# Kernel tuning notes

Measured on AMD Instinct MI355X. Metric: run time of the kernel, lower is better.

The kernel has to match this reference:

```python
import jax, jax.numpy as jnp
import numpy as np
import math

HID = 2048; NH = 16; NKV = 4; NG = NH // NKV
LORA = 512; D_ROPE = 64; D_NOPE = 128; D_V = 128
D_QK = D_NOPE + D_ROPE  # 192
B, S = 2, 2048
ROPE_BASE = 10000.0


def setup_inputs() -> dict:
    key = jax.random.key(0)
    ks = jax.random.split(key, 5)
    s = lambda fan_in: 1.0 / math.sqrt(fan_in)
    return {
        "hidden_states": jax.random.normal(ks[0], (B, S, HID), jnp.float32),
        "Wqkv": jax.random.uniform(ks[1], (HID, NH * D_QK + LORA), jnp.float32, -s(HID), s(HID)),
        "Wk_up": jax.random.uniform(ks[2], (LORA, NKV * D_QK), jnp.float32, -s(LORA), s(LORA)),
        "Wv_up": jax.random.uniform(ks[3], (LORA, NKV * D_V), jnp.float32, -s(LORA), s(LORA)),
        "Wo": jax.random.uniform(ks[4], (NH * D_V, HID), jnp.float32, -s(NH * D_V), s(NH * D_V)),
    }


def _rope(x, seq_len):
    # x: [b, s, h, D_ROPE]; standard rotate-half RoPE
    inv_freq = 1.0 / (ROPE_BASE ** (jnp.arange(0, D_ROPE, 2, dtype=jnp.float32) / D_ROPE))
    t = jnp.arange(seq_len, dtype=jnp.float32)
    freqs = jnp.outer(t, inv_freq)                      # [s, D_ROPE/2]
    emb = jnp.concatenate([freqs, freqs], axis=-1)      # [s, D_ROPE]
    cos = jnp.cos(emb)[None, :, None, :].astype(x.dtype)
    sin = jnp.sin(emb)[None, :, None, :].astype(x.dtype)
    x1, x2 = jnp.split(x, 2, axis=-1)
    rot = jnp.concatenate([-x2, x1], axis=-1)
    return x * cos + rot * sin


def reference(hidden_states, Wqkv, Wk_up, Wv_up, Wo):
    b, s, _ = hidden_states.shape
    qkv = hidden_states @ Wqkv                              # [b,s,NH*D_QK+LORA]
    q, c_kv = jnp.split(qkv, [NH * D_QK], axis=-1)
    q = q.reshape(b, s, NH, D_QK)
    k = (c_kv @ Wk_up).reshape(b, s, NKV, D_QK)
    v = (c_kv @ Wv_up).reshape(b, s, NKV, D_V)
    q_nope, q_rope = jnp.split(q, [D_NOPE], axis=-1)
    k_nope, k_rope = jnp.split(k, [D_NOPE], axis=-1)
    q = jnp.concatenate([q_nope, _rope(q_rope, s)], axis=-1)   # [b,s,NH,D_QK]
    k = jnp.concatenate([k_nope, _rope(k_rope, s)], axis=-1)   # [b,s,NKV,D_QK]
    # GQA broadcast: repeat_interleave kv heads to NH
    k = jnp.repeat(k, NG, axis=2)
    v = jnp.repeat(v, NG, axis=2)
    scale = 1.0 / math.sqrt(D_QK)
    scores = jnp.einsum("bqhd,bkhd->bhqk", q, k) * scale
    causal = jnp.tril(jnp.ones((s, s), bool))
    scores = jnp.where(causal[None, None], scores, jnp.finfo(scores.dtype).min)
    probs = jax.nn.softmax(scores, axis=-1)
    out = jnp.einsum("bhqk,bkhd->bqhd", probs, v).reshape(b, s, NH * D_V)
    return out @ Wo
```

## Files before the change

### kernel.cpp

```cpp
#include <hip/hip_runtime.h>
#include <hip/hip_bf16.h>
#include <math.h>

#define HIDN  2048
#define NH    16
#define NKV   4
#define LORA  512
#define D_ROPE 64
#define D_NOPE 128
#define D_VV  128
#define D_QKD 192
#define BATCH 2
#define SEQ   2048
#define NTOK  (BATCH*SEQ)
#define QKV_W (NH*D_QKD + LORA)
#define KW    (NKV*D_QKD)
#define VW    (NKV*D_VV)
#define AW    (NH*D_VV)
#define QSCALE 0.07216878364870323f
#define LOG2E  1.4426950408889634f

typedef __attribute__((ext_vector_type(8))) __bf16 bf16x8;
typedef __attribute__((ext_vector_type(4))) float f32x4;

static __device__ __forceinline__ unsigned short f2bf(float f) {
    unsigned int u = __builtin_bit_cast(unsigned int, f);
    u += 0x7fffu + ((u >> 16) & 1u);
    return (unsigned short)(u >> 16);
}
static __device__ __forceinline__ float bf2f(unsigned short v) {
    unsigned int u = (unsigned int)v << 16;
    return __builtin_bit_cast(float, u);
}
static __device__ __forceinline__ unsigned int cvt_pk_bf16(float lo, float hi) {
    unsigned int r;
    asm("v_cvt_pk_bf16_f32 %0, %1, %2" : "=v"(r) : "v"(lo), "v"(hi));
    return r;
}
static __device__ __forceinline__ void gl2lds16(const unsigned short* g, unsigned short* l) {
    __builtin_amdgcn_global_load_lds(
        (const __attribute__((address_space(1))) unsigned int*)g,
        (__attribute__((address_space(3))) unsigned int*)l, 16, 0, 0);
}

__global__ __launch_bounds__(256) void transpose_w(
    const float* __restrict__ W, unsigned short* __restrict__ Wt,
    int K, int N, int scale_ncols, float scale)
{
    __shared__ float T[64][68];
    const int tid = threadIdx.x;
    const int k0 = blockIdx.y * 64, n0 = blockIdx.x * 64;
    const int rr = tid >> 4;
    const int c4 = (tid & 15) * 4;

#pragma unroll
    for (int i = 0; i < 4; ++i) {
        int r = rr + 16 * i;
        *(float4*)&T[r][c4] = *(const float4*)&W[(size_t)(k0 + r) * N + n0 + c4];
    }
    __syncthreads();
#pragma unroll
    for (int i = 0; i < 4; ++i) {
        int nr = rr + 16 * i;
        float sc = (n0 + nr < scale_ncols) ? scale : 1.0f;
        unsigned short tmp[4];
#pragma unroll
        for (int j = 0; j < 4; ++j) tmp[j] = f2bf(T[c4 + j][nr] * sc);
        unsigned int p0 = (unsigned int)tmp[0] | ((unsigned int)tmp[1] << 16);
        unsigned int p1 = (unsigned int)tmp[2] | ((unsigned int)tmp[3] << 16);
        *(uint2*)&Wt[(size_t)(n0 + nr) * K + k0 + c4] = make_uint2(p0, p1);
    }
}

__global__ __launch_bounds__(256) void cast_plain(const float* __restrict__ src,
                                                  unsigned short* __restrict__ dst)
{
    int idx = blockIdx.x * 256 + threadIdx.x;
    float4 v = *(const float4*)&src[(size_t)idx * 4];
    unsigned int p0 = (unsigned int)f2bf(v.x) | ((unsigned int)f2bf(v.y) << 16);
    unsigned int p1 = (unsigned int)f2bf(v.z) | ((unsigned int)f2bf(v.w) << 16);
    *(uint2*)&dst[(size_t)idx * 4] = make_uint2(p0, p1);
}

template<int OUT_MODE>
__global__ __launch_bounds__(256) void gemm_bt(
    const unsigned short* __restrict__ A,
    const unsigned short* __restrict__ Bt,
    void* __restrict__ C,
    int K, int lda, int ldb, int ldc)
{
    __shared__ __align__(16) unsigned short As[128 * 32];
    __shared__ __align__(16) unsigned short Bs[128 * 32];

    const int tid  = threadIdx.x;
    const int w    = tid >> 6;
    const int lane = tid & 63;
    const int quad = lane >> 4;
    const int l15  = lane & 15;
    const int brow = blockIdx.y * 128;
    const int bcol = blockIdx.x * 128;
    const int wr   = (w >> 1) * 64;
    const int wc   = (w & 1) * 64;

    const int srow = lane >> 2;
    const int sseg = (lane & 3) * 8;
    const int r0   = w * 32;

    f32x4 acc[4][4];
#pragma unroll
    for (int mt = 0; mt < 4; ++mt)
#pragma unroll
        for (int nt = 0; nt < 4; ++nt) acc[mt][nt] = (f32x4){0.f, 0.f, 0.f, 0.f};

    const unsigned short* Ab = A  + (size_t)(brow + r0 + srow) * lda + sseg;
    const unsigned short* Bb = Bt + (size_t)(bcol + r0 + srow) * ldb + sseg;

    for (int k0 = 0; k0 < K; k0 += 32) {
        __syncthreads();
        gl2lds16(Ab + k0,                     As + r0 * 32);
        gl2lds16(Ab + k0 + (size_t)16 * lda,  As + (r0 + 16) * 32);
        gl2lds16(Bb + k0,                     Bs + r0 * 32);
        gl2lds16(Bb + k0 + (size_t)16 * ldb,  Bs + (r0 + 16) * 32);
        __syncthreads();

        bf16x8 af[4], bfr[4];
#pragma unroll
        for (int mt = 0; mt < 4; ++mt)
            af[mt] = __builtin_bit_cast(bf16x8,
                *(const uint4*)(As + (wr + mt * 16 + l15) * 32 + quad * 8));
#pragma unroll
        for (int nt = 0; nt < 4; ++nt)
            bfr[nt] = __builtin_bit_cast(bf16x8,
                *(const uint4*)(Bs + (wc + nt * 16 + l15) * 32 + quad * 8));
#pragma unroll
        for (int mt = 0; mt < 4; ++mt)
#pragma unroll
            for (int nt = 0; nt < 4; ++nt)
                acc[mt][nt] = __builtin_amdgcn_mfma_f32_16x16x32_bf16(
                    af[mt], bfr[nt], acc[mt][nt], 0, 0, 0);
    }

    if (OUT_MODE == 2) {
#pragma unroll
        for (int mt = 0; mt < 4; ++mt) {
            int row0 = brow + wr + mt * 16 + quad * 4;
            int r5   = row0 & 31;
            int pos  = ((r5 & 15) >> 2) * 8 + ((r5 >> 4) << 2);
            int prow0 = (row0 & ~31) | pos;
#pragma unroll
            for (int nt = 0; nt < 4; ++nt) {
                int col = bcol + wc + nt * 16 + l15;
                unsigned int p0 = (unsigned int)f2bf(acc[mt][nt][0]) |
                                  ((unsigned int)f2bf(acc[mt][nt][1]) << 16);
                unsigned int p1 = (unsigned int)f2bf(acc[mt][nt][2]) |
                                  ((unsigned int)f2bf(acc[mt][nt][3]) << 16);
                *(uint2*)&((unsigned short*)C)[(size_t)col * ldc + prow0] = make_uint2(p0, p1);
            }
        }
    } else {
#pragma unroll
        for (int mt = 0; mt < 4; ++mt)
#pragma unroll
            for (int i = 0; i < 4; ++i) {
                size_t row = (size_t)(brow + wr + mt * 16 + quad * 4 + i);
#pragma unroll
                for (int nt = 0; nt < 4; ++nt) {
                    int col = bcol + wc + nt * 16 + l15;
                    ((unsigned short*)C)[row * ldc + col] = f2bf(acc[mt][nt][i]);
                }
            }
    }
}

template<int OUT_MODE, int BN>
__global__ __launch_bounds__(512, 2) void gemm8p(
    const unsigned short* __restrict__ A,
    const unsigned short* __restrict__ Bt,
    void* __restrict__ C,
    int K, int lda, int ldb, int ldc)
{
    constexpr int BNF = BN / 64;
    constexpr int LB  = BN / 64;
    constexpr int HB  = LB / 2;
    constexpr int ASLOT = 256 * 64;
    constexpr int BSLOT = BN * 64;
    constexpr int SLOT  = ASLOT + BSLOT;
    constexpr int NW  = 3 + 2 * HB;

    extern __shared__ __align__(16) unsigned short lds[];

    const int tid  = threadIdx.x;
    const int w    = tid >> 6;
    const int lane = tid & 63;
    const int quad = lane >> 4;
    const int l15  = lane & 15;
    const int wm   = w >> 2;
    const int wn   = w & 3;

    int fid = blockIdx.y * gridDim.x + blockIdx.x;
    int nwg = gridDim.x * gridDim.y;
    int cpx = nwg >> 3;
    int swz = (fid & 7) * cpx + (fid >> 3);
    int bx  = swz % gridDim.x;
    int by  = swz / gridDim.x;
    const int brow = by * 256;
    const int bcol = bx * BN;

    const unsigned short* Ab = A  + (size_t)brow * lda;
    const unsigned short* Bb = Bt + (size_t)bcol * ldb;

    const int lr   = lane >> 3;
    const int lswz = ((lane & 7) ^ lr) * 8;
    const int arow0 = (w < 4) ? (w * 8) : (128 + (w - 4) * 8);
    const int asrc  = (arow0 + lr) * lda + lswz;
    int brow0[HB], bsrc[HB];
#pragma unroll
    for (int c = 0; c < HB; ++c) {
        brow0[c] = (w * HB + c) * 8;
        bsrc[c]  = (brow0[c] + lr) * ldb + lswz;
    }

    f32x4 acc[8][BNF];
#pragma unroll
    for (int mf = 0; mf < 8; ++mf)
#pragma unroll
        for (int nf = 0; nf < BNF; ++nf) acc[mf][nf] = (f32x4){0.f, 0.f, 0.f, 0.f};

    const int NT = K >> 6;

    auto stageA = [&](int s, int tt, int p) {
        gl2lds16(Ab + tt * 64 + p * 32 * lda + asrc,
                 lds + s * SLOT + (arow0 + p * 32) * 64);
    };
    auto stageB = [&](int s, int tt, int h) {
#pragma unroll
        for (int c = 0; c < HB; ++c)
            gl2lds16(Bb + tt * 64 + h * (BN / 2) * ldb + bsrc[c],
                     lds + s * SLOT + ASLOT + (brow0[c] + h * (BN / 2)) * 64);
    };

    stageB(0, 0, 0); stageB(0, 0, 1);
    stageA(0, 0, 0); stageA(0, 0, 1); stageA(0, 0, 2);
    stageB(1, 1, 0);
    stageA(0, 0, 3);
    stageB(1, 1, 1);
    asm volatile("s_waitcnt vmcnt(%0)" :: "i"(NW) : "memory");
    __builtin_amdgcn_s_barrier();

#pragma unroll 1
    for (int t = 0; t < NT; ++t) {
        const int s  = t & 1;
        const int s1 = s ^ 1;
        const int t1 = (t + 1 < NT) ? t + 1 : 0;
        const int t2 = (t + 2 < NT) ? t + 2 : t + 2 - NT;
        const unsigned short* As = lds + s * SLOT;
        const unsigned short* Bs = As + ASLOT;

        bf16x8 bq[BNF][2], af[2][2];

#pragma unroll
        for (int ph = 0; ph < 4; ++ph) {
            if (ph == 0) {
#pragma unroll
                for (int nf = 0; nf < BNF; ++nf)
#pragma unroll
                    for (int kk = 0; kk < 2; ++kk) {
                        int r = wn * (BN / 4) + nf * 16 + l15;
                        bq[nf][kk] = __builtin_bit_cast(bf16x8,
                            *(const uint4*)(Bs + r * 64 + (((kk * 4 + quad) ^ (r & 7)) * 8)));
                    }
            }
#pragma unroll
            for (int m = 0; m < 2; ++m)
#pragma unroll
                for (int kk = 0; kk < 2; ++kk) {
                    int r = wm * 128 + (ph * 2 + m) * 16 + l15;
                    af[m][kk] = __builtin_bit_cast(bf16x8,
                        *(const uint4*)(As + r * 64 + (((kk * 4 + quad) ^ (r & 7)) * 8)));
                }
            stageA(s1, t1, ph);
            if (ph == 2) stageB(s, t2, 0);
            if (ph == 3) stageB(s, t2, 1);
            __builtin_amdgcn_s_barrier();
            __builtin_amdgcn_s_setprio(1);
#pragma unroll
            for (int m = 0; m < 2; ++m)
#pragma unroll
                for (int nf = 0; nf < BNF; ++nf)
#pragma unroll
                    for (int kk = 0; kk < 2; ++kk)
                        acc[ph * 2 + m][nf] = __builtin_amdgcn_mfma_f32_16x16x32_bf16(
                            af[m][kk], bq[nf][kk], acc[ph * 2 + m][nf], 0, 0, 0);
            __builtin_amdgcn_s_setprio(0);
            asm volatile("s_waitcnt vmcnt(%0)" :: "i"(NW) : "memory");
            __builtin_amdgcn_s_barrier();
        }
    }
    asm volatile("s_waitcnt vmcnt(0)" ::: "memory");

#pragma unroll
    for (int mf = 0; mf < 8; ++mf) {
#pragma unroll
        for (int i = 0; i < 4; ++i) {
            size_t row = (size_t)(brow + wm * 128 + mf * 16 + quad * 4 + i);
#pragma unroll
            for (int nf = 0; nf < BNF; ++nf) {
                int col = bcol + wn * (BN / 4) + nf * 16 + l15;
                if (OUT_MODE == 1)
                    ((unsigned short*)C)[row * ldc + col] = f2bf(acc[mf][nf][i]);
                else
                    ((float*)C)[row * ldc + col] = acc[mf][nf][i];
            }
        }
    }
}

__global__ __launch_bounds__(256) void rope_bf16(unsigned short* __restrict__ qkvb,
                                                 unsigned short* __restrict__ kb)
{
    int idx = blockIdx.x * 256 + threadIdx.x;
    int i    = idx & 31;
    int head = (idx >> 5) % 20;
    int t    = idx / (20 * 32);
    if (t >= NTOK) return;
    int pos = t & (SEQ - 1);

    const float LOG_BASE_OVER_32 = 0.28782313662425572f;
    float ang = (float)pos * __expf(-(float)i * LOG_BASE_OVER_32);
    float c = cosf(ang);
    float sn = sinf(ang);

    unsigned short* p;
    if (head < NH) p = qkvb + (size_t)t * QKV_W + head * D_QKD + D_NOPE;
    else           p = kb   + (size_t)t * KW    + (head - NH) * D_QKD + D_NOPE;

    float x1 = bf2f(p[i]), x2 = bf2f(p[i + 32]);
    p[i]      = f2bf(x1 * c - x2 * sn);
    p[i + 32] = f2bf(x2 * c + x1 * sn);
}

__global__ __launch_bounds__(512) void attn_mfma(
    const unsigned short* __restrict__ qkvb,
    const unsigned short* __restrict__ kb,
    const unsigned short* __restrict__ vt,
    unsigned short* __restrict__ attnb)
{
    __shared__ __align__(16) unsigned short KsL[2 * 32 * 192];
    __shared__ __align__(16) unsigned short VtL[2 * 128 * 32];

    const int tid  = threadIdx.x;
    const int w    = tid >> 6;
    const int lane = tid & 63;
    const int quad = lane >> 4;
    const int l15  = lane & 15;

    const int bid = blockIdx.x;
    const int xcd = bid & 7;
    const int kvh = xcd >> 1;
    const int b   = xcd & 1;
    const int rest = bid >> 3;
    const int h   = kvh * 4 + (rest & 3);
    const int g   = rest >> 2;
    const int qt  = (g < 8) ? (15 - g) : (g - 8);
    const int q0  = qt * 128;

    const int x7   = l15 & 7;
    const int vx   = (l15 >> 1) & 3;

    int koff[2], voff[4];
#pragma unroll
    for (int it = 0; it < 2; ++it) {
        int bidx = ((w - 2) * 2 + it) * 64 + lane;
        int row  = bidx / 24;
        int sblk = bidx - row * 24;
        int gblk = sblk ^ (row & 7);
        koff[it] = row * KW + gblk * 8;
    }
#pragma unroll
    for (int it = 0; it < 4; ++it) {
        int bidx = (w * 4 + it) * 64 + lane;
        int row  = bidx >> 2;
        int gblk = (bidx & 3) ^ ((row >> 1) & 3);
        voff[it] = row * NTOK + gblk * 8;
    }
    const unsigned short* kp0 = kb + (size_t)(b * SEQ) * KW + kvh * D_QKD;
    const unsigned short* vp0 = vt + (size_t)(kvh * 128) * NTOK + b * SEQ;

    const int q0w  = q0 + w * 16;
    const int wmax = q0w + 15;

    bf16x8 qf[6];
    {
        const unsigned short* qp =
            qkvb + (size_t)(b * SEQ + q0w + l15) * QKV_W + h * D_QKD + quad * 8;
#pragma unroll
        for (int t = 0; t < 6; ++t)
            qf[t] = __builtin_bit_cast(bf16x8, *(const uint4*)(qp + t * 32));
    }

    f32x4 o[8];
#pragma unroll
    for (int c = 0; c < 8; ++c) o[c] = (f32x4){0.f, 0.f, 0.f, 0.f};
    float lp = 0.f;

    const int nt = 4 * qt + 4;

    if (w >= 2) {
#pragma unroll
        for (int it = 0; it < 2; ++it)
            gl2lds16(kp0 + koff[it], KsL + ((w - 2) * 2 + it) * 512);
    } else {
#pragma unroll
        for (int it = 0; it < 4; ++it)
            gl2lds16(vp0 + voff[it], VtL + (w * 4 + it) * 512);
    }
    __syncthreads();

    for (int tk = 0; tk < nt; ++tk) {
        const int k0  = tk * 32;
        const int cur = tk & 1;

        if (tk + 1 < nt) {
            const int nxt = cur ^ 1;
            if (w >= 2) {
                const unsigned short* ks = kp0 + (size_t)(k0 + 32) * KW;
#pragma unroll
                for (int it = 0; it < 2; ++it)
                    gl2lds16(ks + koff[it], KsL + nxt * (32 * 192) + ((w - 2) * 2 + it) * 512);
            } else {
                const unsigned short* vs = vp0 + (k0 + 32);
#pragma unroll
                for (int it = 0; it < 4; ++it)
                    gl2lds16(vs + voff[it], VtL + nxt * (128 * 32) + (w * 4 + it) * 512);
            }
        }

        if (k0 <= wmax) {
            const unsigned short* Kc = KsL + cur * (32 * 192);
            const unsigned short* Vc = VtL + cur * (128 * 32);

            f32x4 s[2];
            __builtin_amdgcn_s_setprio(1);
#pragma unroll
            for (int j = 0; j < 2; ++j) {
                f32x4 acc = {0.f, 0.f, 0.f, 0.f};
                const unsigned short* kr = Kc + (j * 16 + l15) * 192;
#pragma unroll
                for (int t = 0; t < 6; ++t) {
                    int sblk = (quad + 4 * t) ^ x7;
                    bf16x8 kf = __builtin_bit_cast(bf16x8, *(const uint4*)(kr + sblk * 8));
                    acc = __builtin_amdgcn_mfma_f32_16x16x32_bf16(kf, qf[t], acc, 0, 0, 0);
                }
                s[j] = acc;
            }
            __builtin_amdgcn_s_setprio(0);

            if (k0 + 31 <= q0w) {
#pragma unroll
                for (int j = 0; j < 2; ++j)
#pragma unroll
                    for (int i = 0; i < 4; ++i) {
                        float p = __builtin_amdgcn_exp2f(s[j][i]);
                        s[j][i] = p;
                        lp += p;
                    }
            } else {
                const int qrow = q0w + l15;
#pragma unroll
                for (int j = 0; j < 2; ++j)
#pragma unroll
                    for (int i = 0; i < 4; ++i) {
                        int kidx = k0 + j * 16 + quad * 4 + i;
                        float p = (kidx <= qrow) ? __builtin_amdgcn_exp2f(s[j][i]) : 0.f;
                        s[j][i] = p;
                        lp += p;
                    }
            }

            uint4 pk;
            pk.x = cvt_pk_bf16(s[0][0], s[0][1]);
            pk.y = cvt_pk_bf16(s[0][2], s[0][3]);
            pk.z = cvt_pk_bf16(s[1][0], s[1][1]);
            pk.w = cvt_pk_bf16(s[1][2], s[1][3]);
            bf16x8 pa = __builtin_bit_cast(bf16x8, pk);

            __builtin_amdgcn_s_setprio(1);
#pragma unroll
            for (int c = 0; c < 8; ++c) {
                bf16x8 vf = __builtin_bit_cast(bf16x8,
                    *(const uint4*)(Vc + (c * 16 + l15) * 32 + ((quad ^ vx) * 8)));
                o[c] = __builtin_amdgcn_mfma_f32_16x16x32_bf16(pa, vf, o[c], 0, 0, 0);
            }
            __builtin_amdgcn_s_setprio(0);
        }

        __syncthreads();
    }

    float lt = lp;
    lt += __shfl_xor(lt, 16);
    lt += __shfl_xor(lt, 32);

#pragma unroll
    for (int i = 0; i < 4; ++i) {
        float inv = 1.0f / __shfl(lt, (lane & 48) | (quad * 4 + i));
        size_t rowoff = (size_t)(b * SEQ + q0w + quad * 4 + i) * AW + h * D_VV + l15;
#pragma unroll
        for (int c = 0; c < 8; ++c)
            attnb[rowoff + c * 16] = f2bf(o[c][i] * inv);
    }
}

extern "C" void kernel_launch(void* const* d_in, const int* in_sizes, int n_in,
                              void* d_out, int out_size, void* d_ws, size_t ws_size,
                              hipStream_t stream)
{
    const float* X     = (const float*)d_in[0];
    const float* Wqkv  = (const float*)d_in[1];
    const float* Wk_up = (const float*)d_in[2];
    const float* Wv_up = (const float*)d_in[3];
    const float* Wo    = (const float*)d_in[4];
    float* out = (float*)d_out;

    unsigned short* Xb    = (unsigned short*)d_ws;
    unsigned short* Wqt   = Xb    + (size_t)NTOK * HIDN;
    unsigned short* Wkt   = Wqt   + (size_t)QKV_W * HIDN;
    unsigned short* Wvt   = Wkt   + (size_t)KW * LORA;
    unsigned short* Wot   = Wvt   + (size_t)VW * LORA;
    unsigned short* qkvb  = Wot   + (size_t)HIDN * AW;
    unsigned short* kb    = qkvb  + (size_t)NTOK * QKV_W;
    unsigned short* vtb   = kb    + (size_t)NTOK * KW;
    unsigned short* attnb = vtb   + (size_t)VW * NTOK;

    cast_plain<<<NTOK * HIDN / 4 / 256, 256, 0, stream>>>(X, Xb);
    transpose_w<<<dim3(QKV_W / 64, HIDN / 64), 256, 0, stream>>>(
        Wqkv, Wqt, HIDN, QKV_W, NH * D_QKD, QSCALE * LOG2E);
    transpose_w<<<dim3(KW / 64, LORA / 64), 256, 0, stream>>>(Wk_up, Wkt, LORA, KW, 0, 1.0f);
    transpose_w<<<dim3(VW / 64, LORA / 64), 256, 0, stream>>>(Wv_up, Wvt, LORA, VW, 0, 1.0f);
    transpose_w<<<dim3(AW / 64, HIDN / 64), 256, 0, stream>>>(Wo, Wot, HIDN, AW, 0, 1.0f);

    gemm8p<1, 256><<<dim3(QKV_W / 256, NTOK / 256), 512, 131072, stream>>>(
        Xb, Wqt, qkvb, HIDN, HIDN, HIDN, QKV_W);

    gemm_bt<1><<<dim3(KW / 128, NTOK / 128), 256, 0, stream>>>(
        qkvb + NH * D_QKD, Wkt, kb, LORA, QKV_W, LORA, KW);
    gemm_bt<2><<<dim3(VW / 128, NTOK / 128), 256, 0, stream>>>(
        qkvb + NH * D_QKD, Wvt, vtb, LORA, QKV_W, LORA, NTOK);

    rope_bf16<<<(NTOK * 20 * 32 + 255) / 256, 256, 0, stream>>>(qkvb, kb);

    attn_mfma<<<dim3(512), 512, 0, stream>>>(qkvb, kb, vtb, attnb);

    gemm8p<0, 128><<<dim3(HIDN / 128, NTOK / 256), 512, 98304, stream>>>(
        attnb, Wot, out, AW, AW, AW, HIDN);
}
```

Before: 326.2 us.

## Restructure GEMM main loop to two barriers per K-tile instead of eight

The per-K-tile loop in the pipelined bf16 GEMM is unrolled by hand into four MFMA phases. Staging of the next A tile is grouped into the first half and the B prefetch into the second half, with a single mid-iteration barrier and one wait-plus-barrier at the end. This replaces two barriers and a vmcnt wait per phase. The aim is to cut workgroup synchronisation stalls between MFMA bursts, at the cost of relying on careful ordering so the in-place B refill of the current slot does not race with reads.

```diff
diff --git a/kernel.cpp b/kernel.cpp
--- a/kernel.cpp
+++ b/kernel.cpp
@@ -180,12 +180,11 @@
     int K, int lda, int ldb, int ldc)
 {
     constexpr int BNF = BN / 64;
-    constexpr int LB  = BN / 64;
-    constexpr int HB  = LB / 2;
+    constexpr int HB  = BN / 128;
+    constexpr int NWT = 2 * HB;
     constexpr int ASLOT = 256 * 64;
     constexpr int BSLOT = BN * 64;
     constexpr int SLOT  = ASLOT + BSLOT;
-    constexpr int NW  = 3 + 2 * HB;
 
     extern __shared__ __align__(16) unsigned short lds[];
 
@@ -240,11 +239,9 @@
     };
 
     stageB(0, 0, 0); stageB(0, 0, 1);
-    stageA(0, 0, 0); stageA(0, 0, 1); stageA(0, 0, 2);
-    stageB(1, 1, 0);
-    stageA(0, 0, 3);
-    stageB(1, 1, 1);
-    asm volatile("s_waitcnt vmcnt(%0)" :: "i"(NW) : "memory");
+    stageA(0, 0, 0); stageA(0, 0, 1); stageA(0, 0, 2); stageA(0, 0, 3);
+    stageB(1, 1, 0); stageB(1, 1, 1);
+    asm volatile("s_waitcnt vmcnt(%0)" :: "i"(NWT) : "memory");
     __builtin_amdgcn_s_barrier();
 
 #pragma unroll 1
@@ -259,42 +256,95 @@
         bf16x8 bq[BNF][2], af[2][2];
 
 #pragma unroll
-        for (int ph = 0; ph < 4; ++ph) {
-            if (ph == 0) {
-#pragma unroll
-                for (int nf = 0; nf < BNF; ++nf)
-#pragma unroll
-                    for (int kk = 0; kk < 2; ++kk) {
-                        int r = wn * (BN / 4) + nf * 16 + l15;
-                        bq[nf][kk] = __builtin_bit_cast(bf16x8,
-                            *(const uint4*)(Bs + r * 64 + (((kk * 4 + quad) ^ (r & 7)) * 8)));
-                    }
-            }
-#pragma unroll
-            for (int m = 0; m < 2; ++m)
-#pragma unroll
-                for (int kk = 0; kk < 2; ++kk) {
-                    int r = wm * 128 + (ph * 2 + m) * 16 + l15;
-                    af[m][kk] = __builtin_bit_cast(bf16x8,
-                        *(const uint4*)(As + r * 64 + (((kk * 4 + quad) ^ (r & 7)) * 8)));
-                }
-            stageA(s1, t1, ph);
-            if (ph == 2) stageB(s, t2, 0);
-            if (ph == 3) stageB(s, t2, 1);
-            __builtin_amdgcn_s_barrier();
-            __builtin_amdgcn_s_setprio(1);
-#pragma unroll
-            for (int m = 0; m < 2; ++m)
-#pragma unroll
-                for (int nf = 0; nf < BNF; ++nf)
-#pragma unroll
-                    for (int kk = 0; kk < 2; ++kk)
-                        acc[ph * 2 + m][nf] = __builtin_amdgcn_mfma_f32_16x16x32_bf16(
-                            af[m][kk], bq[nf][kk], acc[ph * 2 + m][nf], 0, 0, 0);
-            __builtin_amdgcn_s_setprio(0);
-            asm volatile("s_waitcnt vmcnt(%0)" :: "i"(NW) : "memory");
-            __builtin_amdgcn_s_barrier();
-        }
+        for (int nf = 0; nf < BNF; ++nf)
+#pragma unroll
+            for (int kk = 0; kk < 2; ++kk) {
+                int r = wn * (BN / 4) + nf * 16 + l15;
+                bq[nf][kk] = __builtin_bit_cast(bf16x8,
+                    *(const uint4*)(Bs + r * 64 + (((kk * 4 + quad) ^ (r & 7)) * 8)));
+            }
+#pragma unroll
+        for (int m = 0; m < 2; ++m)
+#pragma unroll
+            for (int kk = 0; kk < 2; ++kk) {
+                int r = wm * 128 + m * 16 + l15;
+                af[m][kk] = __builtin_bit_cast(bf16x8,
+                    *(const uint4*)(As + r * 64 + (((kk * 4 + quad) ^ (r & 7)) * 8)));
+            }
+        stageA(s1, t1, 0); stageA(s1, t1, 1);
+        __builtin_amdgcn_s_setprio(1);
+#pragma unroll
+        for (int m = 0; m < 2; ++m)
+#pragma unroll
+            for (int nf = 0; nf < BNF; ++nf)
+#pragma unroll
+                for (int kk = 0; kk < 2; ++kk)
+                    acc[m][nf] = __builtin_amdgcn_mfma_f32_16x16x32_bf16(
+                        af[m][kk], bq[nf][kk], acc[m][nf], 0, 0, 0);
+        __builtin_amdgcn_s_setprio(0);
+
+#pragma unroll
+        for (int m = 0; m < 2; ++m)
+#pragma unroll
+            for (int kk = 0; kk < 2; ++kk) {
+                int r = wm * 128 + (2 + m) * 16 + l15;
+                af[m][kk] = __builtin_bit_cast(bf16x8,
+                    *(const uint4*)(As + r * 64 + (((kk * 4 + quad) ^ (r & 7)) * 8)));
+            }
+        stageA(s1, t1, 2); stageA(s1, t1, 3);
+        __builtin_amdgcn_s_setprio(1);
+#pragma unroll
+        for (int m = 0; m < 2; ++m)
+#pragma unroll
+            for (int nf = 0; nf < BNF; ++nf)
+#pragma unroll
+                for (int kk = 0; kk < 2; ++kk)
+                    acc[2 + m][nf] = __builtin_amdgcn_mfma_f32_16x16x32_bf16(
+                        af[m][kk], bq[nf][kk], acc[2 + m][nf], 0, 0, 0);
+        __builtin_amdgcn_s_setprio(0);
+        __builtin_amdgcn_s_barrier();
+
+#pragma unroll
+        for (int m = 0; m < 2; ++m)
+#pragma unroll
+            for (int kk = 0; kk < 2; ++kk) {
+                int r = wm * 128 + (4 + m) * 16 + l15;
+                af[m][kk] = __builtin_bit_cast(bf16x8,
+                    *(const uint4*)(As + r * 64 + (((kk * 4 + quad) ^ (r & 7)) * 8)));
+            }
+        stageB(s, t2, 0);
+        __builtin_amdgcn_s_setprio(1);
+#pragma unroll
+        for (int m = 0; m < 2; ++m)
+#pragma unroll
+            for (int nf = 0; nf < BNF; ++nf)
+#pragma unroll
+                for (int kk = 0; kk < 2; ++kk)
+                    acc[4 + m][nf] = __builtin_amdgcn_mfma_f32_16x16x32_bf16(
+                        af[m][kk], bq[nf][kk], acc[4 + m][nf], 0, 0, 0);
+        __builtin_amdgcn_s_setprio(0);
+
+#pragma unroll
+        for (int m = 0; m < 2; ++m)
+#pragma unroll
+            for (int kk = 0; kk < 2; ++kk) {
+                int r = wm * 128 + (6 + m) * 16 + l15;
+                af[m][kk] = __builtin_bit_cast(bf16x8,
+                    *(const uint4*)(As + r * 64 + (((kk * 4 + quad) ^ (r & 7)) * 8)));
+            }
+        stageB(s, t2, 1);
+        __builtin_amdgcn_s_setprio(1);
+#pragma unroll
+        for (int m = 0; m < 2; ++m)
+#pragma unroll
+            for (int nf = 0; nf < BNF; ++nf)
+#pragma unroll
+                for (int kk = 0; kk < 2; ++kk)
+                    acc[6 + m][nf] = __builtin_amdgcn_mfma_f32_16x16x32_bf16(
+                        af[m][kk], bq[nf][kk], acc[6 + m][nf], 0, 0, 0);
+        __builtin_amdgcn_s_setprio(0);
+        asm volatile("s_waitcnt vmcnt(%0)" :: "i"(NWT) : "memory");
+        __builtin_amdgcn_s_barrier();
     }
     asm volatile("s_waitcnt vmcnt(0)" ::: "memory");
 
```

Result: faster. 317.8 us (-2.6%).
